# Optimization experiments

Measured on AMD Instinct MI355X. Metric: run time of the kernel, lower is better.

The kernel has to match this reference:

```python
import jax, jax.numpy as jnp
import numpy as np

B, CIN, H, W = 4, 128, 160, 160
K = 100          # num instances
CH = 8           # mask head channels
OUT = 8          # mask branch out channels
STRIDE = 4
EPS = 1e-5


def conv3x3(x, w):
    # x: [B,C,H,W], w: [O,C,3,3] -> [B,O,H,W], stride 1, pad 1
    return jax.lax.conv_general_dilated(x, w, (1, 1), 'SAME',
                                        dimension_numbers=('NCHW', 'OIHW', 'NCHW'))


def setup_inputs() -> dict:
    key = jax.random.key(0)
    ks = jax.random.split(key, 6)
    cnn_feature = jax.random.normal(ks[0], (B, CIN, H, W), jnp.float32)
    tower_w = jax.random.normal(ks[1], (4, 128, 128, 3, 3), jnp.float32) * 0.03
    bn_gamma = jnp.ones((4, 128), jnp.float32)
    bn_beta = jnp.zeros((4, 128), jnp.float32)
    bn_mean = jnp.zeros((4, 128), jnp.float32)
    bn_var = jnp.ones((4, 128), jnp.float32)
    proj_w = jax.random.normal(ks[2], (OUT, 128), jnp.float32) * 0.05
    proj_b = jnp.zeros((OUT,), jnp.float32)
    ctrl_w = jax.random.normal(ks[3], (169, CIN, 3, 3), jnp.float32) * 0.01
    ctrl_b = jnp.zeros((169,), jnp.float32)
    detection = jax.random.randint(ks[4], (K, 2), 0, min(H, W), dtype=jnp.int32)
    return dict(cnn_feature=cnn_feature, tower_w=tower_w, bn_gamma=bn_gamma,
                bn_beta=bn_beta, bn_mean=bn_mean, bn_var=bn_var,
                proj_w=proj_w, proj_b=proj_b, ctrl_w=ctrl_w, ctrl_b=ctrl_b,
                detection=detection)


def reference(cnn_feature, tower_w, bn_gamma, bn_beta, bn_mean, bn_var,
              proj_w, proj_b, ctrl_w, ctrl_b, detection):
    x = cnn_feature
    for i in range(4):
        x = conv3x3(x, tower_w[i])
        inv = bn_gamma[i] / jnp.sqrt(bn_var[i] + EPS)            # [128]
        shift = bn_beta[i] - bn_mean[i] * inv
        x = jax.nn.relu(x * inv[None, :, None, None] + shift[None, :, None, None])
    mask_feats = jnp.einsum('bchw,oc->bohw', x, proj_w) + proj_b[None, :, None, None]

    # ----- controller: 3x3 conv producing 169 dynamic params per pixel -----
    ctrl = conv3x3(cnn_feature, ctrl_w) + ctrl_b[None, :, None, None]  # [B,169,H,W]

    # ----- gather per-instance params at detection centers (im_inds all 0) -----
    xs = detection[:, 0]
    ys = detection[:, 1]
    params = ctrl[0][:, ys, xs].T  # [K,169]

    # ----- relative coordinates -----
    sx = jnp.arange(W, dtype=jnp.float32) * STRIDE + STRIDE // 2
    sy = jnp.arange(H, dtype=jnp.float32) * STRIDE + STRIDE // 2
    gy, gx = jnp.meshgrid(sy, sx, indexing='ij')
    locations = jnp.stack([gx.reshape(-1), gy.reshape(-1)], axis=1)   # [HW,2]
    ct = detection.astype(jnp.float32) * STRIDE                        # [K,2]
    rel = (ct[:, None, :] - locations[None, :, :]).transpose(0, 2, 1)  # [K,2,HW]

    feats = jnp.broadcast_to(mask_feats[0].reshape(1, OUT, H * W), (K, OUT, H * W))
    h = jnp.concatenate([rel, feats], axis=1)  # [K,10,HW]

    # ----- parse dynamic params: weights first, then biases -----
    w0 = params[:, 0:80].reshape(K, CH, OUT + 2)     # (8+2)*8
    w1 = params[:, 80:144].reshape(K, CH, CH)        # 8*8
    w2 = params[:, 144:152].reshape(K, 1, CH)        # 8*1
    b0 = params[:, 152:160]
    b1 = params[:, 160:168]
    b2 = params[:, 168:169]

    # ----- dynamic grouped 1x1 convs == per-instance matmuls -----
    h = jax.nn.relu(jnp.einsum('koc,kcp->kop', w0, h) + b0[:, :, None])
    h = jax.nn.relu(jnp.einsum('koc,kcp->kop', w1, h) + b1[:, :, None])
    h = jnp.einsum('koc,kcp->kop', w2, h) + b2[:, :, None]  # [K,1,HW]
    return h.reshape(K, H, W)
```

## Files before the change

kernel.cpp:

```cpp
#include <hip/hip_runtime.h>
#include <hip/hip_bf16.h>

#define H 160
#define W 160
#define HW 25600
#define ROWB 40960

typedef __attribute__((ext_vector_type(8))) short bf16x8;
typedef __attribute__((ext_vector_type(4))) float f32x4;
typedef __attribute__((ext_vector_type(8))) unsigned short ushort8v;
typedef __attribute__((ext_vector_type(4))) unsigned short ushort4v;

typedef __attribute__((address_space(1))) const unsigned int gu32;
typedef __attribute__((address_space(3))) unsigned int lu32;

__device__ __forceinline__ void gload16(const void* g, void* l) {
    __builtin_amdgcn_global_load_lds((gu32*)g, (lu32*)l, 16, 0, 0);
}

__device__ __forceinline__ unsigned short f2b(float f) {
    unsigned int u = __float_as_uint(f);
    unsigned int r = (u + 0x7fffu + ((u >> 16) & 1u)) >> 16;
    return (unsigned short)r;
}
__device__ __forceinline__ float b2f(unsigned short b) {
    return __uint_as_float(((unsigned int)b) << 16);
}

#define LGKM0() asm volatile("s_waitcnt lgkmcnt(0)" ::: "memory")
#define BARRIER() asm volatile("s_barrier" ::: "memory")


__global__ __launch_bounds__(256) void fused_prep(
    const float* __restrict__ cnn,
    const float* __restrict__ tw,
    const float* __restrict__ gamma, const float* __restrict__ beta,
    const float* __restrict__ mean,  const float* __restrict__ var,
    const float* __restrict__ cw, const float* __restrict__ cb,
    const int*   __restrict__ det,
    char* __restrict__ actX, char* __restrict__ wbf,
    float* __restrict__ invshift, float* __restrict__ params)
{
    const int tid = threadIdx.x;
    const int b = blockIdx.x;

    if (b < 100) {
        __shared__ float patch[1152];
        const int k = b;
        const int xk = det[2 * k];
        const int yk = det[2 * k + 1];
        for (int i = tid; i < 1152; i += 256) {
            int ci = i / 9;
            int rem = i - ci * 9;
            int r = rem / 3, s = rem - r * 3;
            int gy = yk + r - 1, gx = xk + s - 1;
            float v = 0.f;
            if ((unsigned)gy < (unsigned)H && (unsigned)gx < (unsigned)W)
                v = cnn[ci * HW + gy * W + gx];
            patch[i] = v;
        }
        __syncthreads();
        if (tid < 169) {
            float acc = cb[tid];
            const float4* cw4 = (const float4*)&cw[tid * 1152];
            const float4* p4  = (const float4*)patch;
            for (int i = 0; i < 288; ++i) {
                float4 a = p4[i];
                float4 w = cw4[i];
                acc += a.x * w.x + a.y * w.y + a.z * w.z + a.w * w.w;
            }
            params[k * 169 + tid] = acc;
        }
    } else if (b < 1700) {
        int idx = (b - 100) * 256 + tid;
        int cb2 = idx & 15;
        int p  = idx >> 4;
        int x  = p % W;
        int ci0 = cb2 * 8;
        ushort8v o;
#pragma unroll
        for (int j = 0; j < 8; ++j)
            o[j] = f2b(cnn[(ci0 + j) * HW + p]);
        *(ushort8v*)(actX + p * 256 + ((cb2 ^ (x & 15)) * 16)) = o;
    } else {
        int idx = (b - 1700) * 256 + tid;
        int ci = idx & 127;
        int co = (idx >> 7) & 127;
        int l  = idx >> 14;
        int kk = ci >> 5;
        int cw2 = ci & 31;
        const float* src = tw + ((l * 128 + co) * 128 + ci) * 9;
        char* dst = wbf + l * 294912 + kk * 8192 + co * 64 + cw2 * 2;
#pragma unroll
        for (int t = 0; t < 9; ++t)
            *(unsigned short*)(dst + t * 32768) = f2b(src[t]);

        if (b == 1700) {
            for (int c = tid; c < 512; c += 256) {
                int ll = c >> 7, ch = c & 127;
                float inv = gamma[ll * 128 + ch] * rsqrtf(var[ll * 128 + ch] + 1e-5f);
                float sh  = beta[ll * 128 + ch] - mean[ll * 128 + ch] * inv;
                invshift[ll * 256 + ch] = inv;
                invshift[ll * 256 + 128 + ch] = sh;
            }
        }
    }
}

template <int PROJ>
__global__ __launch_bounds__(256, 1) void conv_mfma(
    const char* __restrict__ actin,
    const char* __restrict__ wpl,
    const float* __restrict__ invshift_l,
    char* __restrict__ actout,
    const float* __restrict__ pw,
    const float* __restrict__ pb,
    float* __restrict__ mf)
{
    __shared__ __align__(16) char smem[78848];
    char* IT = smem;
    char* WQ = smem + 46080;

    const int tid  = threadIdx.x;
    const int lane = tid & 63;
    const int w    = tid >> 6;
    const int wc   = w >> 1;
    const int wp   = w & 1;
    const int g    = lane >> 4;
    const int i15  = lane & 15;

    const int bx = blockIdx.x;
    const int by = blockIdx.y;
    const int tx0 = bx * 16 - 1;
    const int ty0 = by * 8 - 1;

    for (int it = 0; it < 12; ++it) {
        int c = it * 256 + tid;
        if (c < 2880) {
            int row  = c / 288;
            int rem  = c - row * 288;
            int px_i = rem >> 4;
            int bo   = (rem & 15) * 16;
            int cy = min(max(ty0 + row, 0), H - 1);
            int cx = min(max(tx0 + px_i, 0), W - 1);
            char* ldsb = IT + (it * 256 + (tid & ~63)) * 16;
            gload16(actin + cy * ROWB + cx * 256 + bo, ldsb);
        }
    }
#pragma unroll
    for (int pl = 0; pl < 3; ++pl) {
        const char* src = wpl + pl * 8192;
        char* dst = WQ + pl * 8192;
        gload16(src + (0 * 256 + tid) * 16, dst + (0 * 256 + (tid & ~63)) * 16);
        gload16(src + (1 * 256 + tid) * 16, dst + (1 * 256 + (tid & ~63)) * 16);
    }
    asm volatile("s_waitcnt vmcnt(6)" ::: "memory");
    for (int c = tid; c < 2880; c += 256) {
        int row  = c / 288;
        int rem  = c - row * 288;
        int px_i = rem >> 4;
        int gy = ty0 + row, gx = tx0 + px_i;
        if ((unsigned)gy >= (unsigned)H || (unsigned)gx >= (unsigned)W) {
            f32x4 z = {0.f, 0.f, 0.f, 0.f};
            *(f32x4*)(IT + c * 16) = z;
        }
    }
    LGKM0();
    BARRIER();

    f32x4 acc[4][4];
#pragma unroll
    for (int cf = 0; cf < 4; ++cf)
#pragma unroll
        for (int pf = 0; pf < 4; ++pf)
            acc[cf][pf] = (f32x4){0.f, 0.f, 0.f, 0.f};

#define CSTAGE(J, WN) {                                                        \
    if ((J) <= 32) {                                                           \
        const char* src = wpl + ((J) + 3) * 8192;                              \
        char* dst = WQ + (((J) + 3) & 3) * 8192;                               \
        gload16(src + (0*256 + tid) * 16, dst + (0*256 + (tid & ~63)) * 16);   \
        gload16(src + (1*256 + tid) * 16, dst + (1*256 + (tid & ~63)) * 16);   \
    }                                                                          \
    asm volatile("s_waitcnt vmcnt(" #WN ")" ::: "memory");                     \
    {                                                                          \
        const int tap = (J) >> 2, kk = (J) & 3;                                \
        const int r = tap / 3, s = tap - r * 3;                                \
        const char* wbse = WQ + ((J) & 3) * 8192 + (wc * 64 + i15) * 64 + g * 16; \
        bf16x8 a0 = *(const bf16x8*)(wbse + 0 * 1024);                         \
        bf16x8 a1 = *(const bf16x8*)(wbse + 1 * 1024);                         \
        bf16x8 a2 = *(const bf16x8*)(wbse + 2 * 1024);                         \
        bf16x8 a3 = *(const bf16x8*)(wbse + 3 * 1024);                         \
        const int slotb = ((kk * 4 + g) ^ ((i15 + s + 15) & 15)) * 16;         \
        const char* ib = IT + (i15 + s) * 256 + slotb;                         \
        bf16x8 b0 = *(const bf16x8*)(ib + (wp * 4 + 0 + r) * 4608);            \
        bf16x8 b1 = *(const bf16x8*)(ib + (wp * 4 + 1 + r) * 4608);            \
        bf16x8 b2 = *(const bf16x8*)(ib + (wp * 4 + 2 + r) * 4608);            \
        bf16x8 b3 = *(const bf16x8*)(ib + (wp * 4 + 3 + r) * 4608);            \
        acc[0][0] = __builtin_amdgcn_mfma_f32_16x16x32_bf16(a0, b0, acc[0][0], 0, 0, 0); \
        acc[0][1] = __builtin_amdgcn_mfma_f32_16x16x32_bf16(a0, b1, acc[0][1], 0, 0, 0); \
        acc[0][2] = __builtin_amdgcn_mfma_f32_16x16x32_bf16(a0, b2, acc[0][2], 0, 0, 0); \
        acc[0][3] = __builtin_amdgcn_mfma_f32_16x16x32_bf16(a0, b3, acc[0][3], 0, 0, 0); \
        acc[1][0] = __builtin_amdgcn_mfma_f32_16x16x32_bf16(a1, b0, acc[1][0], 0, 0, 0); \
        acc[1][1] = __builtin_amdgcn_mfma_f32_16x16x32_bf16(a1, b1, acc[1][1], 0, 0, 0); \
        acc[1][2] = __builtin_amdgcn_mfma_f32_16x16x32_bf16(a1, b2, acc[1][2], 0, 0, 0); \
        acc[1][3] = __builtin_amdgcn_mfma_f32_16x16x32_bf16(a1, b3, acc[1][3], 0, 0, 0); \
        acc[2][0] = __builtin_amdgcn_mfma_f32_16x16x32_bf16(a2, b0, acc[2][0], 0, 0, 0); \
        acc[2][1] = __builtin_amdgcn_mfma_f32_16x16x32_bf16(a2, b1, acc[2][1], 0, 0, 0); \
        acc[2][2] = __builtin_amdgcn_mfma_f32_16x16x32_bf16(a2, b2, acc[2][2], 0, 0, 0); \
        acc[2][3] = __builtin_amdgcn_mfma_f32_16x16x32_bf16(a2, b3, acc[2][3], 0, 0, 0); \
        acc[3][0] = __builtin_amdgcn_mfma_f32_16x16x32_bf16(a3, b0, acc[3][0], 0, 0, 0); \
        acc[3][1] = __builtin_amdgcn_mfma_f32_16x16x32_bf16(a3, b1, acc[3][1], 0, 0, 0); \
        acc[3][2] = __builtin_amdgcn_mfma_f32_16x16x32_bf16(a3, b2, acc[3][2], 0, 0, 0); \
        acc[3][3] = __builtin_amdgcn_mfma_f32_16x16x32_bf16(a3, b3, acc[3][3], 0, 0, 0); \
    }                                                                          \
    BARRIER();                                                                 \
}

    CSTAGE(0,4)  CSTAGE(1,4)  CSTAGE(2,4)  CSTAGE(3,4)  CSTAGE(4,4)  CSTAGE(5,4)
    CSTAGE(6,4)  CSTAGE(7,4)  CSTAGE(8,4)  CSTAGE(9,4)  CSTAGE(10,4) CSTAGE(11,4)
    CSTAGE(12,4) CSTAGE(13,4) CSTAGE(14,4) CSTAGE(15,4) CSTAGE(16,4) CSTAGE(17,4)
    CSTAGE(18,4) CSTAGE(19,4) CSTAGE(20,4) CSTAGE(21,4) CSTAGE(22,4) CSTAGE(23,4)
    CSTAGE(24,4) CSTAGE(25,4) CSTAGE(26,4) CSTAGE(27,4) CSTAGE(28,4) CSTAGE(29,4)
    CSTAGE(30,4) CSTAGE(31,4) CSTAGE(32,4) CSTAGE(33,2) CSTAGE(34,0) CSTAGE(35,0)
#undef CSTAGE

    if (PROJ == 0) {
        const int gx = bx * 16 + i15;
#pragma unroll
        for (int cf = 0; cf < 4; ++cf) {
            int co0 = wc * 64 + cf * 16 + g * 4;
            int cbx = wc * 8 + cf * 2 + (g >> 1);
            int sbyte = ((cbx ^ i15) * 16) + (g & 1) * 8;
            f32x4 inv4 = *(const f32x4*)&invshift_l[co0];
            f32x4 sh4  = *(const f32x4*)&invshift_l[128 + co0];
#pragma unroll
            for (int pf = 0; pf < 4; ++pf) {
                int gy = by * 8 + wp * 4 + pf;
                f32x4 v = acc[cf][pf];
                ushort4v o;
                o.x = f2b(fmaxf(v.x * inv4.x + sh4.x, 0.f));
                o.y = f2b(fmaxf(v.y * inv4.y + sh4.y, 0.f));
                o.z = f2b(fmaxf(v.z * inv4.z + sh4.z, 0.f));
                o.w = f2b(fmaxf(v.w * inv4.w + sh4.w, 0.f));
                *(ushort4v*)(actout + gy * ROWB + gx * 256 + sbyte) = o;
            }
        }
    } else {
        char* actF = smem;
        float* spw = (float*)(smem + 32768);
        __syncthreads();
#pragma unroll
        for (int cf = 0; cf < 4; ++cf) {
            int co0 = wc * 64 + cf * 16 + g * 4;
            int cbx = wc * 8 + cf * 2 + (g >> 1);
            int sbyte = ((cbx ^ i15) * 16) + (g & 1) * 8;
            f32x4 inv4 = *(const f32x4*)&invshift_l[co0];
            f32x4 sh4  = *(const f32x4*)&invshift_l[128 + co0];
#pragma unroll
            for (int pf = 0; pf < 4; ++pf) {
                int px = (wp * 4 + pf) * 16 + i15;
                f32x4 v = acc[cf][pf];
                ushort4v o;
                o.x = f2b(fmaxf(v.x * inv4.x + sh4.x, 0.f));
                o.y = f2b(fmaxf(v.y * inv4.y + sh4.y, 0.f));
                o.z = f2b(fmaxf(v.z * inv4.z + sh4.z, 0.f));
                o.w = f2b(fmaxf(v.w * inv4.w + sh4.w, 0.f));
                *(ushort4v*)(actF + px * 256 + sbyte) = o;
            }
        }
        for (int i = tid; i < 1024; i += 256) spw[i] = pw[i];
        __syncthreads();
        int pxt = tid >> 1;
        int oh  = (tid & 1) * 4;
        float s0 = 0.f, s1 = 0.f, s2 = 0.f, s3 = 0.f;
#pragma unroll
        for (int cb2 = 0; cb2 < 16; ++cb2) {
            ushort8v vv = *(const ushort8v*)(actF + pxt * 256 + ((cb2 ^ (pxt & 15)) * 16));
#pragma unroll
            for (int j = 0; j < 8; ++j) {
                float f = b2f(vv[j]);
                int ci = cb2 * 8 + j;
                s0 += f * spw[(oh + 0) * 128 + ci];
                s1 += f * spw[(oh + 1) * 128 + ci];
                s2 += f * spw[(oh + 2) * 128 + ci];
                s3 += f * spw[(oh + 3) * 128 + ci];
            }
        }
        int p = (by * 8 + (pxt >> 4)) * W + bx * 16 + (pxt & 15);
        mf[(oh + 0) * HW + p] = s0 + pb[oh + 0];
        mf[(oh + 1) * HW + p] = s1 + pb[oh + 1];
        mf[(oh + 2) * HW + p] = s2 + pb[oh + 2];
        mf[(oh + 3) * HW + p] = s3 + pb[oh + 3];
    }
}

__global__ __launch_bounds__(256) void head_kernel(
    const float* __restrict__ mf, const float* __restrict__ params,
    const int* __restrict__ det, float* __restrict__ out)
{
    __shared__ float sp[1690];
    __shared__ int sdet[20];
    const int tid = threadIdx.x;
    const int kg = blockIdx.y;
    for (int i = tid; i < 1690; i += 256) sp[i] = params[kg * 1690 + i];
    if (tid < 20) sdet[tid] = det[kg * 20 + tid];
    __syncthreads();

    const int p = blockIdx.x * 256 + tid;
    const int x = p % W;
    const int y = p / W;
    const float fx = (float)(x * 4 + 2);
    const float fy = (float)(y * 4 + 2);

    float f[8];
#pragma unroll
    for (int o = 0; o < 8; ++o) f[o] = mf[o * HW + p];

#pragma unroll 2
    for (int j = 0; j < 10; ++j) {
        const float* spj = &sp[j * 169];
        const float rel0 = (float)(sdet[2 * j] * 4) - fx;
        const float rel1 = (float)(sdet[2 * j + 1] * 4) - fy;
        float h0[8];
#pragma unroll
        for (int o = 0; o < 8; ++o) {
            float a = spj[152 + o] + spj[o * 10] * rel0 + spj[o * 10 + 1] * rel1;
#pragma unroll
            for (int c = 0; c < 8; ++c) a += spj[o * 10 + 2 + c] * f[c];
            h0[o] = fmaxf(a, 0.f);
        }
        float h1[8];
#pragma unroll
        for (int o = 0; o < 8; ++o) {
            float a = spj[160 + o];
#pragma unroll
            for (int c = 0; c < 8; ++c) a += spj[80 + o * 8 + c] * h0[c];
            h1[o] = fmaxf(a, 0.f);
        }
        float r = spj[168];
#pragma unroll
        for (int c = 0; c < 8; ++c) r += spj[144 + c] * h1[c];
        out[(kg * 10 + j) * HW + p] = r;
    }
}

extern "C" void kernel_launch(void* const* d_in, const int* in_sizes, int n_in,
                              void* d_out, int out_size, void* d_ws, size_t ws_size,
                              hipStream_t stream)
{
    const float* cnn    = (const float*)d_in[0];
    const float* towerw = (const float*)d_in[1];
    const float* gamma  = (const float*)d_in[2];
    const float* beta   = (const float*)d_in[3];
    const float* meanp  = (const float*)d_in[4];
    const float* varp   = (const float*)d_in[5];
    const float* projw  = (const float*)d_in[6];
    const float* projb  = (const float*)d_in[7];
    const float* ctrlw  = (const float*)d_in[8];
    const float* ctrlb  = (const float*)d_in[9];
    const int*   det    = (const int*)d_in[10];
    float* out = (float*)d_out;

    char*  outb     = (char*)d_out;
    char*  X        = outb;
    char*  wbf      = outb + 6553600;
    float* invshift = (float*)(outb + 7733248);

    char*  Y      = (char*)d_ws;
    float* mf     = (float*)((char*)d_ws + 6553600);
    float* params = (float*)((char*)d_ws + 7372800);

    const dim3 blk(256);

    fused_prep<<<dim3(1956), blk, 0, stream>>>(
        cnn, towerw, gamma, beta, meanp, varp, ctrlw, ctrlb, det,
        X, wbf, invshift, params);

    const dim3 cgrid(10, 20);
    conv_mfma<0><<<cgrid, blk, 0, stream>>>(X, wbf + 0 * 294912, invshift + 0 * 256,
                                            Y, nullptr, nullptr, nullptr);
    conv_mfma<0><<<cgrid, blk, 0, stream>>>(Y, wbf + 1 * 294912, invshift + 1 * 256,
                                            X, nullptr, nullptr, nullptr);
    conv_mfma<0><<<cgrid, blk, 0, stream>>>(X, wbf + 2 * 294912, invshift + 2 * 256,
                                            Y, nullptr, nullptr, nullptr);
    conv_mfma<1><<<cgrid, blk, 0, stream>>>(Y, wbf + 3 * 294912, invshift + 3 * 256,
                                            nullptr, projw, projb, mf);

    head_kernel<<<dim3(100, 10), blk, 0, stream>>>(mf, params, det, out);
}
```

Baseline: 117.9 us.

## Double conv block to 512 threads, halve per-wave pixel tile; reorder prep transpose

The tower conv kernel now runs 8 waves per block instead of 4, each holding a 4x2 accumulator tile instead of 4x4. Staging loads and the projection epilogue are spread across twice as many threads. With only 200 blocks on the device, this aims to put more waves per CU to hide MFMA and LDS latency, at the cost of more barrier participants and less register-level reuse of the A fragments. Separately, the prep transpose now assigns one channel group per block so consecutive threads read consecutive pixels, giving coalesced global reads.

```diff
diff --git a/kernel.cpp b/kernel.cpp
--- a/kernel.cpp
+++ b/kernel.cpp
@@ -72,15 +72,15 @@
             params[k * 169 + tid] = acc;
         }
     } else if (b < 1700) {
-        int idx = (b - 100) * 256 + tid;
-        int cb2 = idx & 15;
-        int p  = idx >> 4;
-        int x  = p % W;
+        int j = b - 100;
+        int cb2 = j / 100;
+        int p = (j - cb2 * 100) * 256 + tid;
+        int x = p % W;
         int ci0 = cb2 * 8;
         ushort8v o;
 #pragma unroll
-        for (int j = 0; j < 8; ++j)
-            o[j] = f2b(cnn[(ci0 + j) * HW + p]);
+        for (int jj = 0; jj < 8; ++jj)
+            o[jj] = f2b(cnn[(ci0 + jj) * HW + p]);
         *(ushort8v*)(actX + p * 256 + ((cb2 ^ (x & 15)) * 16)) = o;
     } else {
         int idx = (b - 1700) * 256 + tid;
@@ -108,7 +108,7 @@
 }
 
 template <int PROJ>
-__global__ __launch_bounds__(256, 1) void conv_mfma(
+__global__ __launch_bounds__(512, 1) void conv_mfma(
     const char* __restrict__ actin,
     const char* __restrict__ wpl,
     const float* __restrict__ invshift_l,
@@ -124,8 +124,8 @@
     const int tid  = threadIdx.x;
     const int lane = tid & 63;
     const int w    = tid >> 6;
-    const int wc   = w >> 1;
-    const int wp   = w & 1;
+    const int wp   = w >> 1;
+    const int wc   = w & 1;
     const int g    = lane >> 4;
     const int i15  = lane & 15;
 
@@ -134,8 +134,8 @@
     const int tx0 = bx * 16 - 1;
     const int ty0 = by * 8 - 1;
 
-    for (int it = 0; it < 12; ++it) {
-        int c = it * 256 + tid;
+    for (int it = 0; it < 6; ++it) {
+        int c = it * 512 + tid;
         if (c < 2880) {
             int row  = c / 288;
             int rem  = c - row * 288;
@@ -143,19 +143,16 @@
             int bo   = (rem & 15) * 16;
             int cy = min(max(ty0 + row, 0), H - 1);
             int cx = min(max(tx0 + px_i, 0), W - 1);
-            char* ldsb = IT + (it * 256 + (tid & ~63)) * 16;
+            char* ldsb = IT + (it * 512 + (tid & ~63)) * 16;
             gload16(actin + cy * ROWB + cx * 256 + bo, ldsb);
         }
     }
 #pragma unroll
-    for (int pl = 0; pl < 3; ++pl) {
-        const char* src = wpl + pl * 8192;
-        char* dst = WQ + pl * 8192;
-        gload16(src + (0 * 256 + tid) * 16, dst + (0 * 256 + (tid & ~63)) * 16);
-        gload16(src + (1 * 256 + tid) * 16, dst + (1 * 256 + (tid & ~63)) * 16);
-    }
-    asm volatile("s_waitcnt vmcnt(6)" ::: "memory");
-    for (int c = tid; c < 2880; c += 256) {
+    for (int pl = 0; pl < 3; ++pl)
+        gload16(wpl + pl * 8192 + tid * 16,
+                WQ + pl * 8192 + (tid & ~63) * 16);
+    asm volatile("s_waitcnt vmcnt(2)" ::: "memory");
+    for (int c = tid; c < 2880; c += 512) {
         int row  = c / 288;
         int rem  = c - row * 288;
         int px_i = rem >> 4;
@@ -168,20 +165,17 @@
     LGKM0();
     BARRIER();
 
-    f32x4 acc[4][4];
+    f32x4 acc[4][2];
 #pragma unroll
     for (int cf = 0; cf < 4; ++cf)
 #pragma unroll
-        for (int pf = 0; pf < 4; ++pf)
+        for (int pf = 0; pf < 2; ++pf)
             acc[cf][pf] = (f32x4){0.f, 0.f, 0.f, 0.f};
 
 #define CSTAGE(J, WN) {                                                        \
-    if ((J) <= 32) {                                                           \
-        const char* src = wpl + ((J) + 3) * 8192;                              \
-        char* dst = WQ + (((J) + 3) & 3) * 8192;                               \
-        gload16(src + (0*256 + tid) * 16, dst + (0*256 + (tid & ~63)) * 16);   \
-        gload16(src + (1*256 + tid) * 16, dst + (1*256 + (tid & ~63)) * 16);   \
-    }                                                                          \
+    if ((J) <= 32)                                                             \
+        gload16(wpl + ((J) + 3) * 8192 + tid * 16,                             \
+                WQ + (((J) + 3) & 3) * 8192 + (tid & ~63) * 16);               \
     asm volatile("s_waitcnt vmcnt(" #WN ")" ::: "memory");                     \
     {                                                                          \
         const int tap = (J) >> 2, kk = (J) & 3;                                \
@@ -193,36 +187,26 @@
         bf16x8 a3 = *(const bf16x8*)(wbse + 3 * 1024);                         \
         const int slotb = ((kk * 4 + g) ^ ((i15 + s + 15) & 15)) * 16;         \
         const char* ib = IT + (i15 + s) * 256 + slotb;                         \
-        bf16x8 b0 = *(const bf16x8*)(ib + (wp * 4 + 0 + r) * 4608);            \
-        bf16x8 b1 = *(const bf16x8*)(ib + (wp * 4 + 1 + r) * 4608);            \
-        bf16x8 b2 = *(const bf16x8*)(ib + (wp * 4 + 2 + r) * 4608);            \
-        bf16x8 b3 = *(const bf16x8*)(ib + (wp * 4 + 3 + r) * 4608);            \
+        bf16x8 b0 = *(const bf16x8*)(ib + (wp * 2 + 0 + r) * 4608);            \
+        bf16x8 b1 = *(const bf16x8*)(ib + (wp * 2 + 1 + r) * 4608);            \
         acc[0][0] = __builtin_amdgcn_mfma_f32_16x16x32_bf16(a0, b0, acc[0][0], 0, 0, 0); \
         acc[0][1] = __builtin_amdgcn_mfma_f32_16x16x32_bf16(a0, b1, acc[0][1], 0, 0, 0); \
-        acc[0][2] = __builtin_amdgcn_mfma_f32_16x16x32_bf16(a0, b2, acc[0][2], 0, 0, 0); \
-        acc[0][3] = __builtin_amdgcn_mfma_f32_16x16x32_bf16(a0, b3, acc[0][3], 0, 0, 0); \
         acc[1][0] = __builtin_amdgcn_mfma_f32_16x16x32_bf16(a1, b0, acc[1][0], 0, 0, 0); \
         acc[1][1] = __builtin_amdgcn_mfma_f32_16x16x32_bf16(a1, b1, acc[1][1], 0, 0, 0); \
-        acc[1][2] = __builtin_amdgcn_mfma_f32_16x16x32_bf16(a1, b2, acc[1][2], 0, 0, 0); \
-        acc[1][3] = __builtin_amdgcn_mfma_f32_16x16x32_bf16(a1, b3, acc[1][3], 0, 0, 0); \
         acc[2][0] = __builtin_amdgcn_mfma_f32_16x16x32_bf16(a2, b0, acc[2][0], 0, 0, 0); \
         acc[2][1] = __builtin_amdgcn_mfma_f32_16x16x32_bf16(a2, b1, acc[2][1], 0, 0, 0); \
-        acc[2][2] = __builtin_amdgcn_mfma_f32_16x16x32_bf16(a2, b2, acc[2][2], 0, 0, 0); \
-        acc[2][3] = __builtin_amdgcn_mfma_f32_16x16x32_bf16(a2, b3, acc[2][3], 0, 0, 0); \
         acc[3][0] = __builtin_amdgcn_mfma_f32_16x16x32_bf16(a3, b0, acc[3][0], 0, 0, 0); \
         acc[3][1] = __builtin_amdgcn_mfma_f32_16x16x32_bf16(a3, b1, acc[3][1], 0, 0, 0); \
-        acc[3][2] = __builtin_amdgcn_mfma_f32_16x16x32_bf16(a3, b2, acc[3][2], 0, 0, 0); \
-        acc[3][3] = __builtin_amdgcn_mfma_f32_16x16x32_bf16(a3, b3, acc[3][3], 0, 0, 0); \
     }                                                                          \
     BARRIER();                                                                 \
 }
 
-    CSTAGE(0,4)  CSTAGE(1,4)  CSTAGE(2,4)  CSTAGE(3,4)  CSTAGE(4,4)  CSTAGE(5,4)
-    CSTAGE(6,4)  CSTAGE(7,4)  CSTAGE(8,4)  CSTAGE(9,4)  CSTAGE(10,4) CSTAGE(11,4)
-    CSTAGE(12,4) CSTAGE(13,4) CSTAGE(14,4) CSTAGE(15,4) CSTAGE(16,4) CSTAGE(17,4)
-    CSTAGE(18,4) CSTAGE(19,4) CSTAGE(20,4) CSTAGE(21,4) CSTAGE(22,4) CSTAGE(23,4)
-    CSTAGE(24,4) CSTAGE(25,4) CSTAGE(26,4) CSTAGE(27,4) CSTAGE(28,4) CSTAGE(29,4)
-    CSTAGE(30,4) CSTAGE(31,4) CSTAGE(32,4) CSTAGE(33,2) CSTAGE(34,0) CSTAGE(35,0)
+    CSTAGE(0,2)  CSTAGE(1,2)  CSTAGE(2,2)  CSTAGE(3,2)  CSTAGE(4,2)  CSTAGE(5,2)
+    CSTAGE(6,2)  CSTAGE(7,2)  CSTAGE(8,2)  CSTAGE(9,2)  CSTAGE(10,2) CSTAGE(11,2)
+    CSTAGE(12,2) CSTAGE(13,2) CSTAGE(14,2) CSTAGE(15,2) CSTAGE(16,2) CSTAGE(17,2)
+    CSTAGE(18,2) CSTAGE(19,2) CSTAGE(20,2) CSTAGE(21,2) CSTAGE(22,2) CSTAGE(23,2)
+    CSTAGE(24,2) CSTAGE(25,2) CSTAGE(26,2) CSTAGE(27,2) CSTAGE(28,2) CSTAGE(29,2)
+    CSTAGE(30,2) CSTAGE(31,2) CSTAGE(32,2) CSTAGE(33,1) CSTAGE(34,0) CSTAGE(35,0)
 #undef CSTAGE
 
     if (PROJ == 0) {
@@ -235,8 +219,8 @@
             f32x4 inv4 = *(const f32x4*)&invshift_l[co0];
             f32x4 sh4  = *(const f32x4*)&invshift_l[128 + co0];
 #pragma unroll
-            for (int pf = 0; pf < 4; ++pf) {
-                int gy = by * 8 + wp * 4 + pf;
+            for (int pf = 0; pf < 2; ++pf) {
+                int gy = by * 8 + wp * 2 + pf;
                 f32x4 v = acc[cf][pf];
                 ushort4v o;
                 o.x = f2b(fmaxf(v.x * inv4.x + sh4.x, 0.f));
@@ -258,8 +242,8 @@
             f32x4 inv4 = *(const f32x4*)&invshift_l[co0];
             f32x4 sh4  = *(const f32x4*)&invshift_l[128 + co0];
 #pragma unroll
-            for (int pf = 0; pf < 4; ++pf) {
-                int px = (wp * 4 + pf) * 16 + i15;
+            for (int pf = 0; pf < 2; ++pf) {
+                int px = (wp * 2 + pf) * 16 + i15;
                 f32x4 v = acc[cf][pf];
                 ushort4v o;
                 o.x = f2b(fmaxf(v.x * inv4.x + sh4.x, 0.f));
@@ -269,11 +253,11 @@
                 *(ushort4v*)(actF + px * 256 + sbyte) = o;
             }
         }
-        for (int i = tid; i < 1024; i += 256) spw[i] = pw[i];
+        for (int i = tid; i < 1024; i += 512) spw[i] = pw[i];
         __syncthreads();
-        int pxt = tid >> 1;
-        int oh  = (tid & 1) * 4;
-        float s0 = 0.f, s1 = 0.f, s2 = 0.f, s3 = 0.f;
+        int pxt = tid >> 2;
+        int o0  = (tid & 3) * 2;
+        float s0 = 0.f, s1 = 0.f;
 #pragma unroll
         for (int cb2 = 0; cb2 < 16; ++cb2) {
             ushort8v vv = *(const ushort8v*)(actF + pxt * 256 + ((cb2 ^ (pxt & 15)) * 16));
@@ -281,17 +265,13 @@
             for (int j = 0; j < 8; ++j) {
                 float f = b2f(vv[j]);
                 int ci = cb2 * 8 + j;
-                s0 += f * spw[(oh + 0) * 128 + ci];
-                s1 += f * spw[(oh + 1) * 128 + ci];
-                s2 += f * spw[(oh + 2) * 128 + ci];
-                s3 += f * spw[(oh + 3) * 128 + ci];
+                s0 += f * spw[o0 * 128 + ci];
+                s1 += f * spw[(o0 + 1) * 128 + ci];
             }
         }
         int p = (by * 8 + (pxt >> 4)) * W + bx * 16 + (pxt & 15);
-        mf[(oh + 0) * HW + p] = s0 + pb[oh + 0];
-        mf[(oh + 1) * HW + p] = s1 + pb[oh + 1];
-        mf[(oh + 2) * HW + p] = s2 + pb[oh + 2];
-        mf[(oh + 3) * HW + p] = s3 + pb[oh + 3];
+        mf[o0 * HW + p]       = s0 + pb[o0];
+        mf[(o0 + 1) * HW + p] = s1 + pb[o0 + 1];
     }
 }
 
@@ -371,21 +351,19 @@
     float* mf     = (float*)((char*)d_ws + 6553600);
     float* params = (float*)((char*)d_ws + 7372800);
 
-    const dim3 blk(256);
-
-    fused_prep<<<dim3(1956), blk, 0, stream>>>(
+    fused_prep<<<dim3(1956), dim3(256), 0, stream>>>(
         cnn, towerw, gamma, beta, meanp, varp, ctrlw, ctrlb, det,
         X, wbf, invshift, params);
 
     const dim3 cgrid(10, 20);
-    conv_mfma<0><<<cgrid, blk, 0, stream>>>(X, wbf + 0 * 294912, invshift + 0 * 256,
-                                            Y, nullptr, nullptr, nullptr);
-    conv_mfma<0><<<cgrid, blk, 0, stream>>>(Y, wbf + 1 * 294912, invshift + 1 * 256,
-                                            X, nullptr, nullptr, nullptr);
-    conv_mfma<0><<<cgrid, blk, 0, stream>>>(X, wbf + 2 * 294912, invshift + 2 * 256,
-                                            Y, nullptr, nullptr, nullptr);
-    conv_mfma<1><<<cgrid, blk, 0, stream>>>(Y, wbf + 3 * 294912, invshift + 3 * 256,
-                                            nullptr, projw, projb, mf);
-
-    head_kernel<<<dim3(100, 10), blk, 0, stream>>>(mf, params, det, out);
-}
+    conv_mfma<0><<<cgrid, dim3(512), 0, stream>>>(X, wbf + 0 * 294912, invshift + 0 * 256,
+                                                  Y, nullptr, nullptr, nullptr);
+    conv_mfma<0><<<cgrid, dim3(512), 0, stream>>>(Y, wbf + 1 * 294912, invshift + 1 * 256,
+                                                  X, nullptr, nullptr, nullptr);
+    conv_mfma<0><<<cgrid, dim3(512), 0, stream>>>(X, wbf + 2 * 294912, invshift + 2 * 256,
+                                                  Y, nullptr, nullptr, nullptr);
+    conv_mfma<1><<<cgrid, dim3(512), 0, stream>>>(Y, wbf + 3 * 294912, invshift + 3 * 256,
+                                                  nullptr, projw, projb, mf);
+
+    head_kernel<<<dim3(100, 10), dim3(256), 0, stream>>>(mf, params, det, out);
+}
```

New measurement: 116.7 us. Within noise of the previous version (-1.1%).
